# Optimization experiments

Hardware: AMD Instinct MI355X
Metric: run time of the kernel (lower is better)

## Reference

```python
import jax, jax.numpy as jnp
import numpy as np

N = 6720      # 16 graphs * 420 nodes
E = 33600     # 16 graphs * 2100 edges (5 per node)
DIN = 2048
H1, C1 = 2, 1024   # conv1: heads=2, out=1024 -> concat 2048
H2, C2 = 1, 64     # conv2: heads=1, out=64
ED = 64            # edge_dim
NODES_PER_GRAPH = 420


def _lin(k, fi, fo):
    return jax.random.normal(k, (fi, fo), jnp.float32) / np.sqrt(fi).astype(np.float32)


def setup_inputs() -> dict:
    key = jax.random.key(0)
    ks = jax.random.split(key, 24)
    d = {}
    d["x"] = jax.random.normal(ks[0], (N, DIN), jnp.float32)
    d["edge_index"] = jax.random.randint(ks[1], (2, E), 0, N)
    # tiled learned edge_features param (torch.rand init), one 2100xED block per graph
    ef = jax.random.uniform(ks[2], (5 * NODES_PER_GRAPH, ED), jnp.float32)
    d["edge_attr"] = jnp.tile(ef, (N // NODES_PER_GRAPH, 1))
    HC1 = H1 * C1
    d["q1_w"] = _lin(ks[3], DIN, HC1); d["q1_b"] = jax.random.normal(ks[4], (HC1,)) * 0.01
    d["k1_w"] = _lin(ks[5], DIN, HC1); d["k1_b"] = jax.random.normal(ks[6], (HC1,)) * 0.01
    d["v1_w"] = _lin(ks[7], DIN, HC1); d["v1_b"] = jax.random.normal(ks[8], (HC1,)) * 0.01
    d["e1_w"] = _lin(ks[9], ED, HC1)                      # lin_edge has no bias in PyG
    d["s1_w"] = _lin(ks[10], DIN, HC1); d["s1_b"] = jax.random.normal(ks[11], (HC1,)) * 0.01
    HC2 = H2 * C2
    d["q2_w"] = _lin(ks[12], HC1, HC2); d["q2_b"] = jax.random.normal(ks[13], (HC2,)) * 0.01
    d["k2_w"] = _lin(ks[14], HC1, HC2); d["k2_b"] = jax.random.normal(ks[15], (HC2,)) * 0.01
    d["v2_w"] = _lin(ks[16], HC1, HC2); d["v2_b"] = jax.random.normal(ks[17], (HC2,)) * 0.01
    d["e2_w"] = _lin(ks[18], ED, HC2)
    d["s2_w"] = _lin(ks[19], HC1, HC2); d["s2_b"] = jax.random.normal(ks[20], (HC2,)) * 0.01
    return d


def _transformer_conv(x, src, dst, edge_attr, qw, qb, kw, kb, vw, vb, ew, sw, sb, H, C):
    """PyG TransformerConv (concat=True, beta=False, root_weight=True)."""
    n = x.shape[0]
    q = (x @ qw + qb).reshape(n, H, C)
    k = (x @ kw + kb).reshape(n, H, C)
    v = (x @ vw + vb).reshape(n, H, C)
    e = (edge_attr @ ew).reshape(-1, H, C)         # [E,H,C]
    kj = k[src] + e                                # gather source keys + edge emb
    alpha = jnp.sum(q[dst] * kj, axis=-1) / np.sqrt(C).astype(np.float32)  # [E,H]
    # scatter-softmax over incoming edges of each target node
    amax = jax.ops.segment_max(alpha, dst, num_segments=n)   # [N,H]
    ex = jnp.exp(alpha - amax[dst])
    denom = jax.ops.segment_sum(ex, dst, num_segments=n)
    attn = ex / (denom[dst] + 1e-16)               # [E,H]
    msg = (v[src] + e) * attn[..., None]           # [E,H,C]
    out = jax.ops.segment_sum(msg, dst, num_segments=n).reshape(n, H * C)
    return out + x @ sw + sb                       # root/skip connection


def reference(x, edge_index, edge_attr,
              q1_w, q1_b, k1_w, k1_b, v1_w, v1_b, e1_w, s1_w, s1_b,
              q2_w, q2_b, k2_w, k2_b, v2_w, v2_b, e2_w, s2_w, s2_b):
    src, dst = edge_index[0], edge_index[1]
    h = jax.nn.relu(_transformer_conv(x, src, dst, edge_attr,
                                      q1_w, q1_b, k1_w, k1_b, v1_w, v1_b,
                                      e1_w, s1_w, s1_b, H1, C1))
    h = jax.nn.relu(_transformer_conv(h, src, dst, edge_attr,
                                      q2_w, q2_b, k2_w, k2_b, v2_w, v2_b,
                                      e2_w, s2_w, s2_b, H2, C2))
    return h.reshape(-1, NODES_PER_GRAPH * 64)     # forward returns here (fc layers are dead code)
```

## Files before the change

### kernel.cpp

```cpp
#include <hip/hip_runtime.h>
#include <hip/hip_bf16.h>
#include <cstdint>
#include <cstddef>

#define NN    6720
#define MPAD  6912
#define NE    33600
#define KDIM  2048
#define HC1   2048
#define EAP   2100

typedef __attribute__((ext_vector_type(8))) short bhalf8;
typedef __attribute__((ext_vector_type(4))) short bhalf4;
typedef __attribute__((ext_vector_type(4))) float fx4;

__device__ __forceinline__ float bf2f(short s) {
    union { unsigned int u; float f; } c;
    c.u = ((unsigned int)(unsigned short)s) << 16;
    return c.f;
}

__device__ __forceinline__ void gload16(const __hip_bfloat16* g, void* lds)
{
    __builtin_amdgcn_global_load_lds(
        (const __attribute__((address_space(1))) unsigned int*)g,
        (__attribute__((address_space(3))) unsigned int*)lds,
        16, 0, 0);
}

#define CFENCE asm volatile("" ::: "memory")

__global__ __launch_bounds__(256, 2) void gemm256x128_fused(
    const __hip_bfloat16* __restrict__ A,
    const __hip_bfloat16* __restrict__ Bt,
    const float* __restrict__ bcat,
    __hip_bfloat16* __restrict__ oq,
    __hip_bfloat16* __restrict__ ok,
    __hip_bfloat16* __restrict__ ov,
    float* __restrict__ oh)
{
    __shared__ alignas(16) char Lds[73728];

    const int tid  = threadIdx.x;
    const int w    = tid >> 6;
    const int lane = tid & 63;
    const int wm = w >> 1, wn = w & 1;
    const int sug = ((lane & 3) ^ ((lane >> 3) & 3)) << 3;
    const int rds = (((lane >> 4) ^ (((lane & 15) >> 1) & 3)) << 4);

#define STAGE(T)                                                          \
    { const int s_ = (T) % 3; const int k0_ = (T) * 32;                   \
      char* ab_ = Lds + s_ * 16384 + w * 4096;                            \
      char* bb_ = Lds + 49152 + s_ * 8192 + w * 2048;                     \
      gload16(Ag0 + k0_, ab_);                                            \
      gload16(Ag0 + k0_ + 16 * KDIM, ab_ + 1024);                         \
      gload16(Ag0 + k0_ + 32 * KDIM, ab_ + 2048);                         \
      gload16(Ag0 + k0_ + 48 * KDIM, ab_ + 3072);                         \
      gload16(Bg0 + k0_, bb_);                                            \
      gload16(Bg0 + k0_ + 16 * KDIM, bb_ + 1024); }

#define TILE(T, VM, DOSTAGE)                                              \
    { if (DOSTAGE) { STAGE((T) + 2); }                                    \
      asm volatile("s_waitcnt vmcnt(" VM ")" ::: "memory");               \
      __builtin_amdgcn_s_barrier(); CFENCE;                               \
      const int s_ = (T) % 3;                                             \
      const char* ap_ = Lds + s_ * 16384;                                 \
      const char* bp_ = Lds + 49152 + s_ * 8192;                          \
      bhalf8 af_[8], bf_[4];                                              \
      _Pragma("unroll")                                                   \
      for (int nj = 0; nj < 4; ++nj)                                      \
          bf_[nj] = *(const bhalf8*)(bp_ + (wn * 64 + nj * 16 + (lane & 15)) * 64 + rds); \
      _Pragma("unroll")                                                   \
      for (int mi = 0; mi < 8; ++mi)                                      \
          af_[mi] = *(const bhalf8*)(ap_ + (wm * 128 + mi * 16 + (lane & 15)) * 64 + rds); \
      __builtin_amdgcn_s_setprio(1);                                      \
      _Pragma("unroll")                                                   \
      for (int mi = 0; mi < 8; ++mi)                                      \
          _Pragma("unroll")                                               \
          for (int nj = 0; nj < 4; ++nj)                                  \
              acc[mi][nj] = __builtin_amdgcn_mfma_f32_16x16x32_bf16(      \
                  af_[mi], bf_[nj], acc[mi][nj], 0, 0, 0);                \
      __builtin_amdgcn_s_setprio(0); CFENCE;                              \
      __builtin_amdgcn_s_barrier(); CFENCE; }

    for (int vt = blockIdx.x; vt < 1728; vt += 512) {
        if (vt != (int)blockIdx.x) {
            asm volatile("s_waitcnt vmcnt(0)" ::: "memory");
            __builtin_amdgcn_s_barrier();
            CFENCE;
        }
        const int i0 = vt >> 3;
        const int bx = (vt & 7) * 8 + (i0 & 7);
        const int by = i0 >> 3;
        const int rowA = by * 256;
        const int rowB = bx * 128;
        const __hip_bfloat16* Ag0 = A  + (size_t)(rowA + w * 64 + (lane >> 2)) * KDIM + sug;
        const __hip_bfloat16* Bg0 = Bt + (size_t)(rowB + w * 32 + (lane >> 2)) * KDIM + sug;

        fx4 acc[8][4] = {};

        STAGE(0); STAGE(1);
        for (int t = 0; t < (KDIM / 32) - 2; ++t) {
            TILE(t, "12", 1);
        }
        TILE((KDIM / 32) - 2, "6", 0);
        TILE((KDIM / 32) - 1, "0", 0);

        const int gcol = rowB + wn * 64;
        const int seg  = gcol >> 11;
        const int lcol = gcol & 2047;
        float bv[4];
        #pragma unroll
        for (int nj = 0; nj < 4; ++nj) bv[nj] = bcat[gcol + nj * 16 + (lane & 15)];
        char* scr = Lds + w * 8704;
        const int growA = rowA + wm * 128;

        #pragma unroll
        for (int c = 0; c < 4; ++c) {
            #pragma unroll
            for (int m2 = 0; m2 < 2; ++m2) {
                const int mi = c * 2 + m2;
                #pragma unroll
                for (int nj = 0; nj < 4; ++nj) {
                    const int cl = nj * 16 + (lane & 15);
                    #pragma unroll
                    for (int i2 = 0; i2 < 4; ++i2) {
                        const int rl = m2 * 16 + ((lane >> 4) << 2) + i2;
                        *(float*)(scr + rl * 272 + cl * 4) = acc[mi][nj][i2] + bv[nj];
                    }
                }
            }
            asm volatile("s_waitcnt lgkmcnt(0)" ::: "memory");
            CFENCE;
            const int rrow = (lane >> 4);
            const int u    = lane & 15;
            if (seg < 3) {
                __hip_bfloat16* dst = (seg == 0) ? oq : (seg == 1) ? ok : ov;
                #pragma unroll
                for (int p = 0; p < 8; ++p) {
                    const int row = p * 4 + rrow;
                    const float4 f = *(const float4*)(scr + row * 272 + u * 16);
                    bhalf4 tb;
                    tb[0] = (short)__bfloat16_as_ushort(__float2bfloat16(f.x));
                    tb[1] = (short)__bfloat16_as_ushort(__float2bfloat16(f.y));
                    tb[2] = (short)__bfloat16_as_ushort(__float2bfloat16(f.z));
                    tb[3] = (short)__bfloat16_as_ushort(__float2bfloat16(f.w));
                    *(bhalf4*)&dst[(size_t)(growA + c * 32 + row) * 2048 + lcol + u * 4] = tb;
                }
            } else {
                #pragma unroll
                for (int p = 0; p < 8; ++p) {
                    const int row = p * 4 + rrow;
                    const float4 f = *(const float4*)(scr + row * 272 + u * 16);
                    *(float4*)&oh[(size_t)(growA + c * 32 + row) * 2048 + lcol + u * 4] = f;
                }
            }
            asm volatile("s_waitcnt lgkmcnt(0)" ::: "memory");
            CFENCE;
        }
    }
#undef TILE
#undef STAGE
}

__global__ __launch_bounds__(256) void gemm_bf16(
    const __hip_bfloat16* __restrict__ A,
    const __hip_bfloat16* __restrict__ Bt,
    const float* __restrict__ bias,
    float* __restrict__ C,
    __hip_bfloat16* __restrict__ Cb,
    int M, int N, int K, int flags)
{
    __shared__ alignas(16) __hip_bfloat16 Asm[128 * 64];
    __shared__ alignas(16) __hip_bfloat16 Bsm[128 * 64];
    const int tid  = threadIdx.x;
    const int w    = tid >> 6;
    const int lane = tid & 63;
    const int wr = w >> 1, wc = w & 1;
    const int rowA = blockIdx.y * 128;
    const int rowB = blockIdx.x * 128;
    const int klen = K / gridDim.z;
    const int kbeg = blockIdx.z * klen;

    const int srow = w * 32 + (lane >> 3);
    const int ug8  = ((lane & 7) ^ (lane >> 3)) << 3;
    const __hip_bfloat16* Ag = A  + (size_t)(rowA + srow) * K + ug8;
    const __hip_bfloat16* Bg = Bt + (size_t)(rowB + srow) * K + ug8;
    char* AsBase = (char*)Asm + w * 4096;
    char* BsBase = (char*)Bsm + w * 4096;

    fx4 acc[4][4] = {};

    const int fra = wr * 64 + (lane & 15);
    const int frb = wc * 64 + (lane & 15);
    const int kb  = (lane >> 4) << 4;
    const int swz = (lane & 7) << 4;

    for (int k0 = kbeg; k0 < kbeg + klen; k0 += 64) {
        __syncthreads();
        #pragma unroll
        for (int j = 0; j < 4; ++j) {
            gload16(Ag + (size_t)j * 8 * K + k0, AsBase + j * 1024);
            gload16(Bg + (size_t)j * 8 * K + k0, BsBase + j * 1024);
        }
        __syncthreads();
        #pragma unroll
        for (int kk = 0; kk < 2; ++kk) {
            const int cb = kk * 64 + kb;
            bhalf8 af[4], bfr[4];
            #pragma unroll
            for (int mi = 0; mi < 4; ++mi)
                af[mi] = *(const bhalf8*)((const char*)Asm + (fra + mi * 16) * 128 + (cb ^ swz));
            #pragma unroll
            for (int nj = 0; nj < 4; ++nj)
                bfr[nj] = *(const bhalf8*)((const char*)Bsm + (frb + nj * 16) * 128 + (cb ^ swz));
            #pragma unroll
            for (int mi = 0; mi < 4; ++mi)
                #pragma unroll
                for (int nj = 0; nj < 4; ++nj)
                    acc[mi][nj] = __builtin_amdgcn_mfma_f32_16x16x32_bf16(
                        af[mi], bfr[nj], acc[mi][nj], 0, 0, 0);
        }
    }

    float* Cz = C ? C + (size_t)blockIdx.z * ((size_t)M * N) : nullptr;
    #pragma unroll
    for (int nj = 0; nj < 4; ++nj) {
        const int ccol = rowB + wc * 64 + nj * 16 + (lane & 15);
        const float bv = (flags & 1) ? bias[ccol] : 0.f;
        #pragma unroll
        for (int mi = 0; mi < 4; ++mi) {
            const int crow0 = rowA + wr * 64 + mi * 16 + ((lane >> 4) << 2);
            #pragma unroll
            for (int i = 0; i < 4; ++i) {
                size_t idx = (size_t)(crow0 + i) * N + ccol;
                float v = acc[mi][nj][i] + bv;
                if (flags & 2) v += Cz[idx];
                if (flags & 4) v = fmaxf(v, 0.f);
                if (Cz && !(flags & 8)) Cz[idx] = v;
                if (Cb) Cb[idx] = __float2bfloat16(v);
            }
        }
    }
}

__global__ void reduce4(const float* __restrict__ parts, size_t stride,
                        const float* __restrict__ bias, int colmask,
                        float* __restrict__ dst, int n)
{
    int i = blockIdx.x * 256 + threadIdx.x;
    if (i >= n) return;
    float v = parts[i] + parts[stride + i] + parts[2 * stride + i] + parts[3 * stride + i];
    if (bias) v += bias[i & colmask];
    dst[i] = v;
}

__global__ __launch_bounds__(256) void gemm_tile(
    const float* __restrict__ A, const float* __restrict__ B,
    const float* __restrict__ bias, float* __restrict__ C,
    int M, int N, int K, int flags)
{
    __shared__ float As[16][68];
    __shared__ float Bs[16][64];
    const int tid = threadIdx.x;
    const int bx = blockIdx.x, by = blockIdx.y;
    const int tx = tid & 15, ty = tid >> 4;
    const int arow = tid >> 2, acol = (tid & 3) << 2;
    const int brow = tid >> 4, bcol = (tid & 15) << 2;
    const float* Ag = A + (size_t)(by * 64 + arow) * K + acol;
    const float* Bg = B + (size_t)brow * N + bx * 64 + bcol;
    float acc[4][4] = {};
    for (int k0 = 0; k0 < K; k0 += 16) {
        const float4 av = *(const float4*)(Ag + k0);
        const float4 bv = *(const float4*)(Bg + (size_t)k0 * N);
        __syncthreads();
        As[acol + 0][arow] = av.x;
        As[acol + 1][arow] = av.y;
        As[acol + 2][arow] = av.z;
        As[acol + 3][arow] = av.w;
        *(float4*)&Bs[brow][bcol] = bv;
        __syncthreads();
        #pragma unroll
        for (int kk = 0; kk < 16; ++kk) {
            const float4 a4 = *(const float4*)&As[kk][ty << 2];
            const float4 b4 = *(const float4*)&Bs[kk][tx << 2];
            const float a[4] = {a4.x, a4.y, a4.z, a4.w};
            const float b[4] = {b4.x, b4.y, b4.z, b4.w};
            #pragma unroll
            for (int i = 0; i < 4; ++i)
                #pragma unroll
                for (int j = 0; j < 4; ++j)
                    acc[i][j] += a[i] * b[j];
        }
    }
    const int crow = by * 64 + (ty << 2);
    const int ccol = bx * 64 + (tx << 2);
    float4 b4 = make_float4(0.f, 0.f, 0.f, 0.f);
    if (flags & 1) b4 = *(const float4*)(bias + ccol);
    #pragma unroll
    for (int i = 0; i < 4; ++i) {
        float* cp = C + (size_t)(crow + i) * N + ccol;
        float4 v;
        v.x = acc[i][0] + b4.x; v.y = acc[i][1] + b4.y;
        v.z = acc[i][2] + b4.z; v.w = acc[i][3] + b4.w;
        if (flags & 2) {
            const float4 o = *(const float4*)cp;
            v.x += o.x; v.y += o.y; v.z += o.z; v.w += o.w;
        }
        *(float4*)cp = v;
    }
}

__global__ void count_deg(const int* __restrict__ ei, int* __restrict__ deg)
{
    int e = blockIdx.x * 256 + threadIdx.x;
    if (e < NE) atomicAdd(&deg[ei[NE + e]], 1);
}

__global__ __launch_bounds__(1024) void scan_kernel(const int* __restrict__ deg,
                                                    int* __restrict__ rowptr)
{
    __shared__ int s[1024];
    const int t = threadIdx.x;
    const int base = t * 7;
    int loc[7];
    int sum = 0;
    #pragma unroll
    for (int i = 0; i < 7; ++i) {
        int idx = base + i;
        int v = (idx < NN) ? deg[idx] : 0;
        loc[i] = v; sum += v;
    }
    s[t] = sum;
    __syncthreads();
    for (int off = 1; off < 1024; off <<= 1) {
        int v = (t >= off) ? s[t - off] : 0;
        __syncthreads();
        s[t] += v;
        __syncthreads();
    }
    int running = s[t] - sum;
    #pragma unroll
    for (int i = 0; i < 7; ++i) {
        int idx = base + i;
        if (idx <= NN) rowptr[idx] = running;
        if (idx < NN) running += loc[i];
    }
}

__global__ void fill_csr(const int* __restrict__ ei, const int* __restrict__ rowptr,
                         int* __restrict__ fillctr, int* __restrict__ elist)
{
    int e = blockIdx.x * 256 + threadIdx.x;
    if (e >= NE) return;
    int d = ei[NE + e];
    int pos = atomicAdd(&fillctr[d], 1);
    elist[rowptr[d] + pos] = e;
}

__global__ void sort_csr(const int* __restrict__ rowptr, int* __restrict__ elist)
{
    int n = blockIdx.x * 256 + threadIdx.x;
    if (n >= NN) return;
    int s0 = rowptr[n], s1 = rowptr[n + 1];
    for (int i = s0 + 1; i < s1; ++i) {
        int v = elist[i];
        int j = i - 1;
        while (j >= s0 && elist[j] > v) { elist[j + 1] = elist[j]; --j; }
        elist[j + 1] = v;
    }
}

__global__ void cvt_pad_bf16(const float* __restrict__ src, __hip_bfloat16* __restrict__ dst,
                             int relu)
{
    size_t i = (size_t)(blockIdx.x * 256 + threadIdx.x) * 4;
    int row = (int)(i >> 11);
    float4 v = make_float4(0.f, 0.f, 0.f, 0.f);
    if (row < NN) v = *(const float4*)&src[i];
    if (relu) {
        v.x = fmaxf(v.x, 0.f); v.y = fmaxf(v.y, 0.f);
        v.z = fmaxf(v.z, 0.f); v.w = fmaxf(v.w, 0.f);
    }
    dst[i + 0] = __float2bfloat16(v.x);
    dst[i + 1] = __float2bfloat16(v.y);
    dst[i + 2] = __float2bfloat16(v.z);
    dst[i + 3] = __float2bfloat16(v.w);
}

__global__ __launch_bounds__(256) void transpose_cvt4(
    const float* __restrict__ W0, const float* __restrict__ W1,
    const float* __restrict__ W2, const float* __restrict__ W3,
    __hip_bfloat16* __restrict__ dst)
{
    const float* W = (blockIdx.z == 0) ? W0 : (blockIdx.z == 1) ? W1
                   : (blockIdx.z == 2) ? W2 : W3;
    __hip_bfloat16* Bt = dst + (size_t)blockIdx.z * KDIM * KDIM;
    __shared__ float t[32][33];
    int kb = blockIdx.y * 32, nb = blockIdx.x * 32;
    int tx = threadIdx.x & 31, ty = threadIdx.x >> 5;
    #pragma unroll
    for (int i = 0; i < 32; i += 8)
        t[ty + i][tx] = W[(size_t)(kb + ty + i) * KDIM + nb + tx];
    __syncthreads();
    #pragma unroll
    for (int i = 0; i < 32; i += 8)
        Bt[(size_t)(nb + ty + i) * KDIM + kb + tx] = __float2bfloat16(t[tx][ty + i]);
}

__global__ void build_bcat(const float* __restrict__ q1b, const float* __restrict__ k1b,
                           const float* __restrict__ v1b, const float* __restrict__ s1b,
                           float* __restrict__ bcat)
{
    int i = blockIdx.x * 256 + threadIdx.x;
    if (i >= 4 * KDIM) return;
    int seg = i >> 11, j = i & 2047;
    const float* b = (seg == 0) ? q1b : (seg == 1) ? k1b : (seg == 2) ? v1b : s1b;
    bcat[i] = b[j];
}

__global__ void build_w1pp(const float* __restrict__ e1w, __hip_bfloat16* __restrict__ w1pp)
{
    int idx = blockIdx.x * 256 + threadIdx.x;
    int p = idx >> 11, j = idx & 2047;
    float v = ((j >> 10) == (p >> 6)) ? e1w[(size_t)(p & 63) * KDIM + j] : 0.f;
    w1pp[idx] = __float2bfloat16(v);
}

__global__ void build_w1ppT(const float* __restrict__ e1w, __hip_bfloat16* __restrict__ w1ppT)
{
    int idx = blockIdx.x * 256 + threadIdx.x;
    int n = idx >> 7, k = idx & 127;
    float v = ((n >> 10) == (k >> 6)) ? e1w[(size_t)(k & 63) * KDIM + n] : 0.f;
    w1ppT[idx] = __float2bfloat16(v);
}

__global__ void build_w2t(const float* __restrict__ qw, const float* __restrict__ kw,
                          const float* __restrict__ vw, const float* __restrict__ sw,
                          const float* __restrict__ qb, const float* __restrict__ kb,
                          const float* __restrict__ vb, const float* __restrict__ sb,
                          __hip_bfloat16* __restrict__ w2t, float* __restrict__ b2)
{
    int idx = blockIdx.x * 256 + threadIdx.x;
    int c = idx >> 11, d = idx & 2047;
    int g = c >> 6, j = c & 63;
    const float* w = (g == 0) ? qw : (g == 1) ? kw : (g == 2) ? vw : sw;
    w2t[idx] = __float2bfloat16(w[(size_t)d * 64 + j]);
    if (d == 0) {
        const float* b = (g == 0) ? qb : (g == 1) ? kb : (g == 2) ? vb : sb;
        b2[c] = b[j];
    }
}

__global__ __launch_bounds__(256) void node1_kernel(
    const __hip_bfloat16* __restrict__ q1b, const __hip_bfloat16* __restrict__ k1b,
    const __hip_bfloat16* __restrict__ v1b,
    const float* __restrict__ P1, const float* __restrict__ ea,
    const int* __restrict__ ei, const int* __restrict__ rowptr,
    const int* __restrict__ elist,
    float* __restrict__ h1, __hip_bfloat16* __restrict__ R1)
{
    __shared__ int   s_src[256];
    __shared__ int   s_em[256];
    __shared__ float s_at[256][2];
    const int n = blockIdx.x;
    const int s0 = rowptr[n];
    const int deg = rowptr[n + 1] - s0;
    const int w = threadIdx.x >> 6, lane = threadIdx.x & 63;

    for (int j = w; j < deg; j += 4) {
        const int e = elist[s0 + j];
        const int src = ei[e];
        const int em = e % EAP;
        if (lane == 0) { s_src[j] = src; s_em[j] = em; }
        const float eaj = ea[(size_t)em * 64 + lane];
        #pragma unroll
        for (int h = 0; h < 2; ++h) {
            const __hip_bfloat16* qh = q1b + (size_t)n * HC1 + h * 1024 + lane * 16;
            const __hip_bfloat16* kh = k1b + (size_t)src * HC1 + h * 1024 + lane * 16;
            bhalf8 qa = *(const bhalf8*)qh, qc = *(const bhalf8*)(qh + 8);
            bhalf8 ka = *(const bhalf8*)kh, kc = *(const bhalf8*)(kh + 8);
            float s = 0.f;
            #pragma unroll
            for (int jj = 0; jj < 8; ++jj) s += bf2f(qa[jj]) * bf2f(ka[jj]);
            #pragma unroll
            for (int jj = 0; jj < 8; ++jj) s += bf2f(qc[jj]) * bf2f(kc[jj]);
            s += eaj * P1[(size_t)n * 128 + h * 64 + lane];
            #pragma unroll
            for (int off = 32; off; off >>= 1) s += __shfl_xor(s, off);
            if (lane == 0) s_at[j][h] = s * 0.03125f;
        }
    }
    __syncthreads();

    if (threadIdx.x < 2) {
        const int h = threadIdx.x;
        float m = -1e30f;
        for (int j = 0; j < deg; ++j) m = fmaxf(m, s_at[j][h]);
        float sum = 0.f;
        for (int j = 0; j < deg; ++j) {
            float ex = __expf(s_at[j][h] - m);
            s_at[j][h] = ex; sum += ex;
        }
        float inv = 1.f / (sum + 1e-16f);
        for (int j = 0; j < deg; ++j) s_at[j][h] *= inv;
    }
    __syncthreads();

    if (threadIdx.x < 128) {
        const int h = threadIdx.x >> 6, jj = threadIdx.x & 63;
        float r = 0.f;
        for (int j = 0; j < deg; ++j)
            r += s_at[j][h] * ea[(size_t)s_em[j] * 64 + jj];
        R1[(size_t)n * 128 + threadIdx.x] = __float2bfloat16(r);
    }

    const int c0 = threadIdx.x * 8;
    const int h = c0 >> 10;
    float acc[8];
    const float4 p0 = *(const float4*)&h1[(size_t)n * HC1 + c0];
    const float4 p1 = *(const float4*)&h1[(size_t)n * HC1 + c0 + 4];
    acc[0] = p0.x; acc[1] = p0.y; acc[2] = p0.z; acc[3] = p0.w;
    acc[4] = p1.x; acc[5] = p1.y; acc[6] = p1.z; acc[7] = p1.w;
    for (int j = 0; j < deg; ++j) {
        const float at = s_at[j][h];
        bhalf8 v = *(const bhalf8*)&v1b[(size_t)s_src[j] * HC1 + c0];
        #pragma unroll
        for (int jj = 0; jj < 8; ++jj) acc[jj] += at * bf2f(v[jj]);
    }
    *(float4*)&h1[(size_t)n * HC1 + c0]     = make_float4(acc[0], acc[1], acc[2], acc[3]);
    *(float4*)&h1[(size_t)n * HC1 + c0 + 4] = make_float4(acc[4], acc[5], acc[6], acc[7]);
}

__global__ __launch_bounds__(64) void node2_kernel(
    const float* __restrict__ qkvs2, const float* __restrict__ E2s,
    const int* __restrict__ ei, const int* __restrict__ rowptr,
    const int* __restrict__ elist, float* __restrict__ out)
{
    __shared__ float s_at[256];
    __shared__ int   s_src[256];
    __shared__ int   s_em[256];
    const int n = blockIdx.x;
    const int s0 = rowptr[n];
    const int deg = rowptr[n + 1] - s0;
    const int c = threadIdx.x;
    const float q = qkvs2[(size_t)n * 256 + c];

    for (int j = 0; j < deg; ++j) {
        const int e = elist[s0 + j];
        const int src = ei[e];
        const int em = e % EAP;
        float s = q * (qkvs2[(size_t)src * 256 + 64 + c] + E2s[(size_t)em * 64 + c]);
        #pragma unroll
        for (int off = 32; off; off >>= 1) s += __shfl_xor(s, off);
        if (c == 0) { s_at[j] = s * 0.125f; s_src[j] = src; s_em[j] = em; }
    }
    __syncthreads();
    float m = -1e30f;
    for (int j = 0; j < deg; ++j) m = fmaxf(m, s_at[j]);
    float sum = 0.f;
    for (int j = 0; j < deg; ++j) sum += __expf(s_at[j] - m);
    const float inv = 1.f / (sum + 1e-16f);

    float acc = qkvs2[(size_t)n * 256 + 192 + c];
    for (int j = 0; j < deg; ++j) {
        const float at = __expf(s_at[j] - m) * inv;
        acc += at * (qkvs2[(size_t)s_src[j] * 256 + 128 + c] + E2s[(size_t)s_em[j] * 64 + c]);
    }
    out[(size_t)n * 64 + c] = fmaxf(acc, 0.f);
}

extern "C" void kernel_launch(void* const* d_in, const int* in_sizes, int n_in,
                              void* d_out, int out_size, void* d_ws, size_t ws_size,
                              hipStream_t stream)
{
    const float* x   = (const float*)d_in[0];
    const int*   ei  = (const int*)d_in[1];
    const float* ea  = (const float*)d_in[2];
    const float* q1w = (const float*)d_in[3];
    const float* q1b = (const float*)d_in[4];
    const float* k1w = (const float*)d_in[5];
    const float* k1b = (const float*)d_in[6];
    const float* v1w = (const float*)d_in[7];
    const float* v1b = (const float*)d_in[8];
    const float* e1w = (const float*)d_in[9];
    const float* s1w = (const float*)d_in[10];
    const float* s1b = (const float*)d_in[11];
    const float* q2w = (const float*)d_in[12];
    const float* q2b = (const float*)d_in[13];
    const float* k2w = (const float*)d_in[14];
    const float* k2b = (const float*)d_in[15];
    const float* v2w = (const float*)d_in[16];
    const float* v2b = (const float*)d_in[17];
    const float* e2w = (const float*)d_in[18];
    const float* s2w = (const float*)d_in[19];
    const float* s2b = (const float*)d_in[20];
    float* out = (float*)d_out;

    char* base = (char*)d_ws;
    size_t off = 0;
    auto alloc = [&](size_t nbytes) {
        size_t o = off; off += (nbytes + 255) & ~(size_t)255; return o;
    };
    const size_t xb_off   = alloc((size_t)MPAD * KDIM * 2);
    const size_t wcat_off = alloc((size_t)4 * KDIM * KDIM * 2);
    __hip_bfloat16* xb    = (__hip_bfloat16*)(base + xb_off);
    __hip_bfloat16* wcat  = (__hip_bfloat16*)(base + wcat_off);
    __hip_bfloat16* h1b   = xb;
    float*          Cpart = (float*)(base + wcat_off);
    __hip_bfloat16* w2t   = (__hip_bfloat16*)(base + wcat_off + (size_t)29 * 1024 * 1024);

    __hip_bfloat16* q1bb  = (__hip_bfloat16*)(base + alloc((size_t)MPAD * HC1 * 2));
    __hip_bfloat16* k1bb  = (__hip_bfloat16*)(base + alloc((size_t)MPAD * HC1 * 2));
    __hip_bfloat16* v1bb  = (__hip_bfloat16*)(base + alloc((size_t)MPAD * HC1 * 2));
    float*          h1    = (float*)(base + alloc((size_t)MPAD * HC1 * 4));
    float*          bcat  = (float*)(base + alloc((size_t)4 * KDIM * 4));
    float*          P1    = (float*)(base + alloc((size_t)MPAD * 128 * 4));
    __hip_bfloat16* R1b   = (__hip_bfloat16*)(base + alloc((size_t)MPAD * 128 * 2));
    __hip_bfloat16* w1pp  = (__hip_bfloat16*)(base + alloc((size_t)128 * KDIM * 2));
    __hip_bfloat16* w1ppT = (__hip_bfloat16*)(base + alloc((size_t)KDIM * 128 * 2));
    float*          b2    = (float*)(base + alloc(256 * 4));
    float*          qkvs2 = (float*)(base + alloc((size_t)MPAD * 256 * 4));
    float*          E2s   = (float*)(base + alloc((size_t)2112 * 64 * 4));
    int* deg    = (int*)(base + alloc((size_t)NN * 4));
    int* fill   = (int*)(base + alloc((size_t)NN * 4));
    int* rowptr = (int*)(base + alloc((size_t)(NN + 1) * 4));
    int* elist  = (int*)(base + alloc((size_t)NE * 4));

    hipMemsetAsync(deg, 0, sizeof(int) * 2 * NN, stream);
    count_deg<<<(NE + 255) / 256, 256, 0, stream>>>(ei, deg);
    scan_kernel<<<1, 1024, 0, stream>>>(deg, rowptr);
    fill_csr<<<(NE + 255) / 256, 256, 0, stream>>>(ei, rowptr, fill, elist);
    sort_csr<<<(NN + 255) / 256, 256, 0, stream>>>(rowptr, elist);

    const int cvblk = (MPAD * KDIM / 4) / 256;
    cvt_pad_bf16<<<cvblk, 256, 0, stream>>>(x, xb, 0);
    transpose_cvt4<<<dim3(KDIM / 32, KDIM / 32, 4), 256, 0, stream>>>(q1w, k1w, v1w, s1w, wcat);
    build_bcat<<<(4 * KDIM) / 256, 256, 0, stream>>>(q1b, k1b, v1b, s1b, bcat);
    build_w1pp<<<(128 * KDIM) / 256, 256, 0, stream>>>(e1w, w1pp);
    build_w1ppT<<<(KDIM * 128) / 256, 256, 0, stream>>>(e1w, w1ppT);
    gemm_tile<<<dim3(1, 33), 256, 0, stream>>>(ea, e2w, nullptr, E2s, 2112, 64, 64, 0);

    gemm256x128_fused<<<512, 256, 0, stream>>>(xb, wcat, bcat, q1bb, k1bb, v1bb, h1);

    gemm_bf16<<<dim3(1, MPAD / 128, 4), 256, 0, stream>>>(q1bb, w1pp, nullptr, Cpart, nullptr,
                                                          MPAD, 128, KDIM, 0);
    reduce4<<<(MPAD * 128) / 256, 256, 0, stream>>>(Cpart, (size_t)MPAD * 128, nullptr, 0,
                                                    P1, MPAD * 128);

    node1_kernel<<<NN, 256, 0, stream>>>(q1bb, k1bb, v1bb, P1, ea, ei, rowptr, elist, h1, R1b);
    gemm_bf16<<<dim3(HC1 / 128, MPAD / 128), 256, 0, stream>>>(R1b, w1ppT, nullptr, h1, h1b,
                                                               MPAD, HC1, 128, 2 | 4 | 8);

    build_w2t<<<(256 * KDIM) / 256, 256, 0, stream>>>(q2w, k2w, v2w, s2w, q2b, k2b, v2b, s2b,
                                                      w2t, b2);
    gemm_bf16<<<dim3(2, MPAD / 128, 4), 256, 0, stream>>>(h1b, w2t, nullptr, Cpart, nullptr,
                                                          MPAD, 256, KDIM, 0);
    reduce4<<<(MPAD * 256) / 256, 256, 0, stream>>>(Cpart, (size_t)MPAD * 256, b2, 255,
                                                    qkvs2, MPAD * 256);

    node2_kernel<<<NN, 64, 0, stream>>>(qkvs2, E2s, ei, rowptr, elist, out);

    (void)in_sizes; (void)n_in; (void)out_size; (void)ws_size;
}
```

Measured before the change: 486.5 us.

## Rewrite fused QKVS GEMM as 256x256 tile with 8-wave four-phase pipeline

Replaces the persistent 256x128, 4-wave, triple-buffered QKVS projection GEMM with a non-persistent 256x256 tile kernel using 8 waves (512 threads), BK=64 and double-buffered LDS of 128 KB. Global-to-LDS loads for the next K-tile are split into four quarter-stages interleaved with four MFMA phases separated by barriers, so loads overlap compute. The larger tile raises arithmetic intensity per byte loaded. In exchange it uses much more LDS per block, which likely limits occupancy to one block per CU despite the launch bound. It also adds more barriers per K-step and launches 864 blocks instead of a grid-stride loop.

```diff
diff --git a/kernel.cpp b/kernel.cpp
--- a/kernel.cpp
+++ b/kernel.cpp
@@ -30,7 +30,7 @@
 
 #define CFENCE asm volatile("" ::: "memory")
 
-__global__ __launch_bounds__(256, 2) void gemm256x128_fused(
+__global__ __launch_bounds__(512, 2) void gemm256_8ph(
     const __hip_bfloat16* __restrict__ A,
     const __hip_bfloat16* __restrict__ Bt,
     const float* __restrict__ bcat,
@@ -39,128 +39,152 @@
     __hip_bfloat16* __restrict__ ov,
     float* __restrict__ oh)
 {
-    __shared__ alignas(16) char Lds[73728];
+    __shared__ alignas(16) char Lds[131072];
+
+    const int bid = blockIdx.x;
+    const int i0  = bid >> 3;
+    const int bx  = (bid & 7) * 4 + (i0 & 3);
+    const int by  = i0 >> 2;
 
     const int tid  = threadIdx.x;
     const int w    = tid >> 6;
     const int lane = tid & 63;
-    const int wm = w >> 1, wn = w & 1;
-    const int sug = ((lane & 3) ^ ((lane >> 3) & 3)) << 3;
-    const int rds = (((lane >> 4) ^ (((lane & 15) >> 1) & 3)) << 4);
-
-#define STAGE(T)                                                          \
-    { const int s_ = (T) % 3; const int k0_ = (T) * 32;                   \
-      char* ab_ = Lds + s_ * 16384 + w * 4096;                            \
-      char* bb_ = Lds + 49152 + s_ * 8192 + w * 2048;                     \
-      gload16(Ag0 + k0_, ab_);                                            \
-      gload16(Ag0 + k0_ + 16 * KDIM, ab_ + 1024);                         \
-      gload16(Ag0 + k0_ + 32 * KDIM, ab_ + 2048);                         \
-      gload16(Ag0 + k0_ + 48 * KDIM, ab_ + 3072);                         \
-      gload16(Bg0 + k0_, bb_);                                            \
-      gload16(Bg0 + k0_ + 16 * KDIM, bb_ + 1024); }
-
-#define TILE(T, VM, DOSTAGE)                                              \
-    { if (DOSTAGE) { STAGE((T) + 2); }                                    \
-      asm volatile("s_waitcnt vmcnt(" VM ")" ::: "memory");               \
-      __builtin_amdgcn_s_barrier(); CFENCE;                               \
-      const int s_ = (T) % 3;                                             \
-      const char* ap_ = Lds + s_ * 16384;                                 \
-      const char* bp_ = Lds + 49152 + s_ * 8192;                          \
-      bhalf8 af_[8], bf_[4];                                              \
-      _Pragma("unroll")                                                   \
-      for (int nj = 0; nj < 4; ++nj)                                      \
-          bf_[nj] = *(const bhalf8*)(bp_ + (wn * 64 + nj * 16 + (lane & 15)) * 64 + rds); \
-      _Pragma("unroll")                                                   \
-      for (int mi = 0; mi < 8; ++mi)                                      \
-          af_[mi] = *(const bhalf8*)(ap_ + (wm * 128 + mi * 16 + (lane & 15)) * 64 + rds); \
-      __builtin_amdgcn_s_setprio(1);                                      \
-      _Pragma("unroll")                                                   \
-      for (int mi = 0; mi < 8; ++mi)                                      \
-          _Pragma("unroll")                                               \
-          for (int nj = 0; nj < 4; ++nj)                                  \
-              acc[mi][nj] = __builtin_amdgcn_mfma_f32_16x16x32_bf16(      \
-                  af_[mi], bf_[nj], acc[mi][nj], 0, 0, 0);                \
-      __builtin_amdgcn_s_setprio(0); CFENCE;                              \
-      __builtin_amdgcn_s_barrier(); CFENCE; }
-
-    for (int vt = blockIdx.x; vt < 1728; vt += 512) {
-        if (vt != (int)blockIdx.x) {
-            asm volatile("s_waitcnt vmcnt(0)" ::: "memory");
-            __builtin_amdgcn_s_barrier();
-            CFENCE;
-        }
-        const int i0 = vt >> 3;
-        const int bx = (vt & 7) * 8 + (i0 & 7);
-        const int by = i0 >> 3;
-        const int rowA = by * 256;
-        const int rowB = bx * 128;
-        const __hip_bfloat16* Ag0 = A  + (size_t)(rowA + w * 64 + (lane >> 2)) * KDIM + sug;
-        const __hip_bfloat16* Bg0 = Bt + (size_t)(rowB + w * 32 + (lane >> 2)) * KDIM + sug;
-
-        fx4 acc[8][4] = {};
-
-        STAGE(0); STAGE(1);
-        for (int t = 0; t < (KDIM / 32) - 2; ++t) {
-            TILE(t, "12", 1);
-        }
-        TILE((KDIM / 32) - 2, "6", 0);
-        TILE((KDIM / 32) - 1, "0", 0);
-
-        const int gcol = rowB + wn * 64;
-        const int seg  = gcol >> 11;
-        const int lcol = gcol & 2047;
-        float bv[4];
-        #pragma unroll
-        for (int nj = 0; nj < 4; ++nj) bv[nj] = bcat[gcol + nj * 16 + (lane & 15)];
-        char* scr = Lds + w * 8704;
-        const int growA = rowA + wm * 128;
-
-        #pragma unroll
-        for (int c = 0; c < 4; ++c) {
-            #pragma unroll
-            for (int m2 = 0; m2 < 2; ++m2) {
-                const int mi = c * 2 + m2;
+    const int wm = w >> 2, wn = w & 3;
+    const int l15 = lane & 15;
+    const int rowA = by * 256;
+    const int rowB = bx * 256;
+
+    const int sug = ((lane & 7) ^ (lane >> 3)) << 3;
+    const __hip_bfloat16* Agb = A  + (size_t)(rowA + w * 16 + (lane >> 3)) * KDIM + sug;
+    const __hip_bfloat16* Bgb = Bt + (size_t)(rowB + w * 16 + (lane >> 3)) * KDIM + sug;
+
+    const int uk0 = (((lane >> 4)    ) ^ (lane & 7)) << 4;
+    const int uk1 = (((lane >> 4) + 4) ^ (lane & 7)) << 4;
+
+    fx4 acc[8][4] = {};
+
+#define STAGE_A(T, H)                                                      \
+    { char* dst_ = Lds + ((T) & 1) * 32768 + (H) * 16384 + (w * 16) * 128; \
+      const __hip_bfloat16* g_ = Agb + (size_t)((H) * 128) * KDIM + (size_t)(T) * 64; \
+      gload16(g_, dst_);                                                   \
+      gload16(g_ + 8 * KDIM, dst_ + 1024); }
+
+#define STAGE_B(T, H)                                                      \
+    { char* dst_ = Lds + 65536 + ((T) & 1) * 32768 + (H) * 16384 + (w * 16) * 128; \
+      const __hip_bfloat16* g_ = Bgb + (size_t)((H) * 128) * KDIM + (size_t)(T) * 64; \
+      gload16(g_, dst_);                                                   \
+      gload16(g_ + 8 * KDIM, dst_ + 1024); }
+
+#define PH_READ_AF(q)                                                      \
+    _Pragma("unroll")                                                      \
+    for (int m2 = 0; m2 < 2; ++m2) {                                       \
+        const char* rp_ = Ab + (((q) * 2 + m2) * 16 + l15) * 128;          \
+        af[m2][0] = *(const bhalf8*)(rp_ + uk0);                           \
+        af[m2][1] = *(const bhalf8*)(rp_ + uk1);                           \
+    }
+
+#define PH_MFMA(q)                                                         \
+    __builtin_amdgcn_s_setprio(1);                                         \
+    _Pragma("unroll")                                                      \
+    for (int m2 = 0; m2 < 2; ++m2)                                         \
+        _Pragma("unroll")                                                  \
+        for (int nj = 0; nj < 4; ++nj)                                     \
+            _Pragma("unroll")                                              \
+            for (int kk = 0; kk < 2; ++kk)                                 \
+                acc[(q) * 2 + m2][nj] = __builtin_amdgcn_mfma_f32_16x16x32_bf16( \
+                    af[m2][kk], bf[nj][kk], acc[(q) * 2 + m2][nj], 0, 0, 0); \
+    __builtin_amdgcn_s_setprio(0);
+
+    STAGE_A(0, 0); STAGE_B(0, 0); STAGE_A(0, 1); STAGE_B(0, 1);
+
+    for (int T = 0; T < 32; ++T) {
+        const char* Ab = Lds + (T & 1) * 32768 + wm * 16384;
+        const char* Bb = Lds + 65536 + (T & 1) * 32768 + (wn >> 1) * 16384;
+        bhalf8 bf[4][2], af[2][2];
+
+        if (T < 31) { STAGE_A(T + 1, 0); }
+        if (T < 31) { asm volatile("s_waitcnt vmcnt(2)" ::: "memory"); }
+        else        { asm volatile("s_waitcnt vmcnt(0)" ::: "memory"); }
+        __builtin_amdgcn_s_barrier(); CFENCE;
+        #pragma unroll
+        for (int nj = 0; nj < 4; ++nj) {
+            const char* rp_ = Bb + ((wn & 1) * 64 + nj * 16 + l15) * 128;
+            bf[nj][0] = *(const bhalf8*)(rp_ + uk0);
+            bf[nj][1] = *(const bhalf8*)(rp_ + uk1);
+        }
+        PH_READ_AF(0);
+        PH_MFMA(0);
+        CFENCE; __builtin_amdgcn_s_barrier(); CFENCE;
+        if (T < 31) { STAGE_B(T + 1, 0); }
+        PH_READ_AF(1);
+        PH_MFMA(1);
+        CFENCE; __builtin_amdgcn_s_barrier(); CFENCE;
+        if (T < 31) { STAGE_A(T + 1, 1); }
+        PH_READ_AF(2);
+        PH_MFMA(2);
+        CFENCE; __builtin_amdgcn_s_barrier(); CFENCE;
+        if (T < 31) { STAGE_B(T + 1, 1); }
+        PH_READ_AF(3);
+        PH_MFMA(3);
+        CFENCE; __builtin_amdgcn_s_barrier(); CFENCE;
+    }
+#undef PH_MFMA
+#undef PH_READ_AF
+#undef STAGE_B
+#undef STAGE_A
+
+    const int gcol = rowB + wn * 64;
+    const int seg  = gcol >> 11;
+    const int lcol = gcol & 2047;
+    float bv[4];
+    #pragma unroll
+    for (int nj = 0; nj < 4; ++nj) bv[nj] = bcat[gcol + nj * 16 + l15];
+    char* scr = Lds + w * 8704;
+    const int growA = rowA + wm * 128;
+
+    #pragma unroll
+    for (int c = 0; c < 4; ++c) {
+        #pragma unroll
+        for (int m2 = 0; m2 < 2; ++m2) {
+            const int mi = c * 2 + m2;
+            #pragma unroll
+            for (int nj = 0; nj < 4; ++nj) {
+                const int cl = nj * 16 + l15;
                 #pragma unroll
-                for (int nj = 0; nj < 4; ++nj) {
-                    const int cl = nj * 16 + (lane & 15);
-                    #pragma unroll
-                    for (int i2 = 0; i2 < 4; ++i2) {
-                        const int rl = m2 * 16 + ((lane >> 4) << 2) + i2;
-                        *(float*)(scr + rl * 272 + cl * 4) = acc[mi][nj][i2] + bv[nj];
-                    }
+                for (int i2 = 0; i2 < 4; ++i2) {
+                    const int rl = m2 * 16 + ((lane >> 4) << 2) + i2;
+                    *(float*)(scr + rl * 272 + cl * 4) = acc[mi][nj][i2] + bv[nj];
                 }
             }
-            asm volatile("s_waitcnt lgkmcnt(0)" ::: "memory");
-            CFENCE;
-            const int rrow = (lane >> 4);
-            const int u    = lane & 15;
-            if (seg < 3) {
-                __hip_bfloat16* dst = (seg == 0) ? oq : (seg == 1) ? ok : ov;
-                #pragma unroll
-                for (int p = 0; p < 8; ++p) {
-                    const int row = p * 4 + rrow;
-                    const float4 f = *(const float4*)(scr + row * 272 + u * 16);
-                    bhalf4 tb;
-                    tb[0] = (short)__bfloat16_as_ushort(__float2bfloat16(f.x));
-                    tb[1] = (short)__bfloat16_as_ushort(__float2bfloat16(f.y));
-                    tb[2] = (short)__bfloat16_as_ushort(__float2bfloat16(f.z));
-                    tb[3] = (short)__bfloat16_as_ushort(__float2bfloat16(f.w));
-                    *(bhalf4*)&dst[(size_t)(growA + c * 32 + row) * 2048 + lcol + u * 4] = tb;
-                }
-            } else {
-                #pragma unroll
-                for (int p = 0; p < 8; ++p) {
-                    const int row = p * 4 + rrow;
-                    const float4 f = *(const float4*)(scr + row * 272 + u * 16);
-                    *(float4*)&oh[(size_t)(growA + c * 32 + row) * 2048 + lcol + u * 4] = f;
-                }
+        }
+        asm volatile("s_waitcnt lgkmcnt(0)" ::: "memory");
+        CFENCE;
+        const int rrow = (lane >> 4);
+        const int u    = lane & 15;
+        if (seg < 3) {
+            __hip_bfloat16* dst = (seg == 0) ? oq : (seg == 1) ? ok : ov;
+            #pragma unroll
+            for (int p = 0; p < 8; ++p) {
+                const int row = p * 4 + rrow;
+                const float4 f = *(const float4*)(scr + row * 272 + u * 16);
+                bhalf4 tb;
+                tb[0] = (short)__bfloat16_as_ushort(__float2bfloat16(f.x));
+                tb[1] = (short)__bfloat16_as_ushort(__float2bfloat16(f.y));
+                tb[2] = (short)__bfloat16_as_ushort(__float2bfloat16(f.z));
+                tb[3] = (short)__bfloat16_as_ushort(__float2bfloat16(f.w));
+                *(bhalf4*)&dst[(size_t)(growA + c * 32 + row) * 2048 + lcol + u * 4] = tb;
             }
-            asm volatile("s_waitcnt lgkmcnt(0)" ::: "memory");
-            CFENCE;
-        }
-    }
-#undef TILE
-#undef STAGE
+        } else {
+            #pragma unroll
+            for (int p = 0; p < 8; ++p) {
+                const int row = p * 4 + rrow;
+                const float4 f = *(const float4*)(scr + row * 272 + u * 16);
+                *(float4*)&oh[(size_t)(growA + c * 32 + row) * 2048 + lcol + u * 4] = f;
+            }
+        }
+        asm volatile("s_waitcnt lgkmcnt(0)" ::: "memory");
+        CFENCE;
+    }
 }
 
 __global__ __launch_bounds__(256) void gemm_bf16(
@@ -641,7 +665,7 @@
     build_w1ppT<<<(KDIM * 128) / 256, 256, 0, stream>>>(e1w, w1ppT);
     gemm_tile<<<dim3(1, 33), 256, 0, stream>>>(ea, e2w, nullptr, E2s, 2112, 64, 64, 0);
 
-    gemm256x128_fused<<<512, 256, 0, stream>>>(xb, wcat, bcat, q1bb, k1bb, v1bb, h1);
+    gemm256_8ph<<<864, 512, 0, stream>>>(xb, wcat, bcat, q1bb, k1bb, v1bb, h1);
 
     gemm_bf16<<<dim3(1, MPAD / 128, 4), 256, 0, stream>>>(q1bb, w1pp, nullptr, Cpart, nullptr,
                                                           MPAD, 128, KDIM, 0);
```

After: 483.4 us. About the same (-0.6%).
